# Kernel tuning notes

Measured on AMD Instinct MI355X. Metric: run time of the kernel, lower is better.

The kernel has to match this reference:

```python
import jax, jax.numpy as jnp
import numpy as np
from jax import lax

B, N, S, NS = 2, 16384, 4096, 32  # batch, points, fps samples, neighbors per ball
RADIUS = 0.08
C_IN = 64
MLP_DIMS = [3 + C_IN, 64, 64, 128]


def setup_inputs() -> dict:
    key = jax.random.key(0)
    ks = jax.random.split(key, 8)
    xyz = jax.random.uniform(ks[0], (B, N, 3), jnp.float32)  # unit cube point cloud
    features = jax.random.normal(ks[1], (B, C_IN, N), jnp.float32)
    inp = {"xyz": xyz, "features": features}
    for i in range(3):
        inp[f"W{i}"] = jax.random.normal(ks[2 + i], (MLP_DIMS[i + 1], MLP_DIMS[i]), jnp.float32) * 0.05
        inp[f"b{i}"] = jnp.zeros((MLP_DIMS[i + 1],), jnp.float32)
    return inp


def _furthest_point_sample(xyz, npoint):
    # Iterative FPS, vectorized over batch; sequential over npoint via lax.scan.
    b, n, _ = xyz.shape
    init_idx = jnp.zeros((b,), jnp.int32)

    def step(carry, _):
        min_d, last_idx = carry
        last = jnp.take_along_axis(xyz, last_idx[:, None, None], axis=1)  # (B,1,3)
        d = jnp.sum((xyz - last) ** 2, axis=-1)  # (B,N)
        min_d = jnp.minimum(min_d, d)
        nxt = jnp.argmax(min_d, axis=-1).astype(jnp.int32)
        return (min_d, nxt), nxt

    init_d = jnp.full((b, n), 1e10, xyz.dtype)
    _, rest = lax.scan(step, (init_d, init_idx), None, length=npoint - 1)
    return jnp.concatenate([init_idx[None, :], rest], axis=0).T  # (B, npoint)


def _ball_query(xyz, new_xyz, radius, nsample):
    # For each query, the first `nsample` points (by index order) within radius,
    # padded with the first found index (matches CUDA ball_query semantics).
    n = xyz.shape[1]
    d2 = jnp.sum((new_xyz[:, :, None, :] - xyz[:, None, :, :]) ** 2, axis=-1)  # (B,S,N)
    valid = d2 < radius * radius
    cnt = valid.sum(axis=-1)  # (B,S)
    keyidx = jnp.where(valid, jnp.arange(n, dtype=jnp.int32), n)
    _, idx = lax.top_k(-keyidx, nsample)  # smallest valid indices first
    idx = idx.astype(jnp.int32)
    slot_valid = jnp.arange(nsample) < cnt[..., None]
    idx = jnp.where(slot_valid, idx, idx[..., :1])
    return idx, cnt


def reference(xyz, features, W0, b0, W1, b1, W2, b2):
    fps_idx = _furthest_point_sample(xyz, S)  # (B,S)
    new_xyz = jnp.take_along_axis(xyz, fps_idx[..., None], axis=1)  # (B,S,3)

    idx, cnt = _ball_query(xyz, new_xyz, RADIUS, NS)  # (B,S,NS), (B,S)
    grouped_xyz = jax.vmap(lambda p, i: p[i])(xyz, idx)  # (B,S,NS,3)
    rel = (grouped_xyz - new_xyz[:, :, None, :]).transpose(0, 3, 1, 2)  # (B,3,S,NS)
    grouped_feat = jax.vmap(lambda f, i: f[:, i])(features, idx)  # (B,C,S,NS)
    x = jnp.concatenate([rel, grouped_feat], axis=1)  # (B,3+C,S,NS)

    for W, b in ((W0, b0), (W1, b1), (W2, b2)):  # shared MLP = 1x1 conv + ReLU
        x = jax.nn.relu(jnp.einsum('oc,bcsn->bosn', W, x) + b[None, :, None, None])

    mask = (cnt > 0).astype(x.dtype)[:, None, :, None]  # zero out empty balls
    x = x * mask
    new_features = x.max(axis=-1)  # masked max-pool over neighbors -> (B,128,S)
    return new_xyz, new_features
```

## Files before the change

### kernel.cpp

```cpp
#include <hip/hip_runtime.h>

#pragma clang fp contract(off)

#define BATCH 2
#define NPTS  16384
#define SS    4096
#define NSAMP 32
#define CIN   64

__global__ __launch_bounds__(256) void prep_kernel(
    const float* __restrict__ feat, const float* __restrict__ W0,
    float* __restrict__ ftr, float* __restrict__ W0p)
{
    __shared__ float tl[64][65];
    const int t = threadIdx.x;
    const int blk = blockIdx.x;
    if (blk < BATCH * (NPTS / 64)) {
        const int b  = blk / (NPTS / 64);
        const int n0 = (blk % (NPTS / 64)) * 64;
        #pragma unroll
        for (int k = 0; k < 16; ++k) {
            int c = k * 4 + (t >> 6);
            int n = t & 63;
            tl[c][n] = feat[((size_t)b * CIN + c) * NPTS + n0 + n];
        }
        __syncthreads();
        #pragma unroll
        for (int k = 0; k < 16; ++k) {
            int n = k * 4 + (t >> 6);
            int c = t & 63;
            ftr[((size_t)b * NPTS + n0 + n) * CIN + c] = tl[c][n];
        }
    } else {
        for (int i = t; i < 64 * 68; i += 256) {
            int r = i / 68, c = i % 68;
            W0p[i] = (c < 67) ? W0[r * 67 + c] : 0.f;
        }
    }
}

__global__ __launch_bounds__(1024, 4) void fps_kernel(
    const float* __restrict__ xyz, float* __restrict__ newxyz)
{
    #pragma clang fp contract(off)
    const int b = blockIdx.x;
    const int t = threadIdx.x;
    const float* xb = xyz + (size_t)b * NPTS * 3;

    float px[16], py[16], pz[16], md[16];
    #pragma unroll
    for (int k = 0; k < 16; ++k) {
        int p = (k << 10) + t;
        px[k] = xb[p * 3 + 0];
        py[k] = xb[p * 3 + 1];
        pz[k] = xb[p * 3 + 2];
        md[k] = 1e10f;
    }

    __shared__ float2 s_w[2][16];

    float lx = xb[0], ly = xb[1], lz = xb[2];
    if (t == 0) {
        float* o = newxyz + (size_t)b * SS * 3;
        o[0] = lx; o[1] = ly; o[2] = lz;
    }

    for (int s = 1; s < SS; ++s) {
        float bv = -1.f;
        int bi = 0;
        #pragma unroll
        for (int k = 0; k < 16; ++k) {
            float dx = px[k] - lx, dy = py[k] - ly, dz = pz[k] - lz;
            float d = (dx * dx + dy * dy) + dz * dz;
            float m = md[k];
            m = d < m ? d : m;
            md[k] = m;
            if (m > bv) { bv = m; bi = (k << 10) + t; }
        }

        #pragma unroll
        for (int m = 1; m < 64; m <<= 1) {
            float ov = __shfl_xor(bv, m);
            int   oi = __shfl_xor(bi, m);
            bool take = (ov > bv) || (ov == bv && oi < bi);
            if (take) { bv = ov; bi = oi; }
        }

        const int pb = s & 1;
        if ((t & 63) == 0)
            s_w[pb][t >> 6] = make_float2(bv, __int_as_float(bi));
        __syncthreads();

        float2 rw = s_w[pb][t & 15];
        float rv = rw.x;
        int   ri = __float_as_int(rw.y);
        #pragma unroll
        for (int m = 1; m < 16; m <<= 1) {
            float ov = __shfl_xor(rv, m);
            int   oi = __shfl_xor(ri, m);
            bool take = (ov > rv) || (ov == rv && oi < ri);
            if (take) { rv = ov; ri = oi; }
        }

        const int wi = __builtin_amdgcn_readfirstlane(ri);
        lx = xb[wi * 3 + 0];
        ly = xb[wi * 3 + 1];
        lz = xb[wi * 3 + 2];
        if (t == 0) {
            float* o = newxyz + ((size_t)b * SS + s) * 3;
            o[0] = lx; o[1] = ly; o[2] = lz;
        }
    }
}

__global__ __launch_bounds__(256) void bq_kernel(
    const float* __restrict__ xyz, const float* __restrict__ newxyz,
    int* __restrict__ idxout, int* __restrict__ cntout)
{
    #pragma clang fp contract(off)
    const int lane = threadIdx.x & 63;
    const int q = blockIdx.x * 4 + (threadIdx.x >> 6);
    const int b = q >> 12;
    const float r2 = (float)(0.08 * 0.08);
    const float cx = newxyz[q * 3 + 0];
    const float cy = newxyz[q * 3 + 1];
    const float cz = newxyz[q * 3 + 2];
    const float* xb = xyz + (size_t)b * NPTS * 3;

    int found = 0;
    int idx0 = 0;
    for (int base = 0; base < NPTS; base += 64) {
        int p = base + lane;
        float dx = xb[p * 3 + 0] - cx;
        float dy = xb[p * 3 + 1] - cy;
        float dz = xb[p * 3 + 2] - cz;
        float d2 = (dx * dx + dy * dy) + dz * dz;
        bool valid = d2 < r2;
        unsigned long long mask = __ballot(valid);
        if (mask) {
            if (found == 0) idx0 = base + (__ffsll(mask) - 1);
            int rank = found + __popcll(mask & ((1ull << lane) - 1ull));
            if (valid && rank < NSAMP) idxout[(size_t)q * NSAMP + rank] = p;
            found += (int)__popcll(mask);
            if (found >= NSAMP) break;
        }
    }
    if (found < NSAMP) {
        int pad = (found > 0) ? idx0 : 0;
        if (found + lane < NSAMP) idxout[(size_t)q * NSAMP + found + lane] = pad;
    }
    if (lane == 0) cntout[q] = found;
}

__global__ __launch_bounds__(128) void mlp_kernel(
    const float* __restrict__ xyz, const float* __restrict__ newxyz,
    const float* __restrict__ ftr, const int* __restrict__ idxbuf,
    const int* __restrict__ cntbuf, const float* __restrict__ W0p,
    const float* __restrict__ b0, const float* __restrict__ W1,
    const float* __restrict__ b1, const float* __restrict__ W2,
    const float* __restrict__ b2, float* __restrict__ outfeat)
{
    __shared__ float sX[2][68 * 36];
    __shared__ float sY[2][64 * 36];
    const int w    = threadIdx.x >> 6;
    const int lane = threadIdx.x & 63;
    const int g = blockIdx.x * 2 + w;
    const int b = g >> 12;
    const int s = g & (SS - 1);
    float* X = sX[w];
    float* Y = sY[w];

    const int n = lane & 31, h = lane >> 5;
    const int pidx = idxbuf[(size_t)g * NSAMP + n];
    const float cx = newxyz[g * 3 + 0];
    const float cy = newxyz[g * 3 + 1];
    const float cz = newxyz[g * 3 + 2];

    if (h == 0) {
        const float* p = xyz + ((size_t)b * NPTS + pidx) * 3;
        X[0 * 36 + n] = p[0] - cx;
        X[1 * 36 + n] = p[1] - cy;
        X[2 * 36 + n] = p[2] - cz;
        X[67 * 36 + n] = 0.f;
    }
    {
        const float4* f4 = (const float4*)(ftr + ((size_t)b * NPTS + pidx) * CIN + h * 32);
        #pragma unroll
        for (int j = 0; j < 8; ++j) {
            float4 v = f4[j];
            int c = 3 + h * 32 + j * 4;
            X[(c + 0) * 36 + n] = v.x;
            X[(c + 1) * 36 + n] = v.y;
            X[(c + 2) * 36 + n] = v.z;
            X[(c + 3) * 36 + n] = v.w;
        }
    }
    __syncthreads();

    const int og = lane >> 3, ng = lane & 7;

    float acc0[8][4];
    #pragma unroll
    for (int j = 0; j < 8; ++j)
        #pragma unroll
        for (int nn = 0; nn < 4; ++nn) acc0[j][nn] = 0.f;
    for (int cb = 0; cb < 17; ++cb) {
        const int c = cb * 4;
        float4 xr0 = *(const float4*)&X[(c + 0) * 36 + ng * 4];
        float4 xr1 = *(const float4*)&X[(c + 1) * 36 + ng * 4];
        float4 xr2 = *(const float4*)&X[(c + 2) * 36 + ng * 4];
        float4 xr3 = *(const float4*)&X[(c + 3) * 36 + ng * 4];
        #pragma unroll
        for (int j = 0; j < 8; ++j) {
            float4 wv = *(const float4*)&W0p[(size_t)(og * 8 + j) * 68 + c];
            acc0[j][0] = fmaf(wv.x, xr0.x, acc0[j][0]);
            acc0[j][1] = fmaf(wv.x, xr0.y, acc0[j][1]);
            acc0[j][2] = fmaf(wv.x, xr0.z, acc0[j][2]);
            acc0[j][3] = fmaf(wv.x, xr0.w, acc0[j][3]);
            acc0[j][0] = fmaf(wv.y, xr1.x, acc0[j][0]);
            acc0[j][1] = fmaf(wv.y, xr1.y, acc0[j][1]);
            acc0[j][2] = fmaf(wv.y, xr1.z, acc0[j][2]);
            acc0[j][3] = fmaf(wv.y, xr1.w, acc0[j][3]);
            acc0[j][0] = fmaf(wv.z, xr2.x, acc0[j][0]);
            acc0[j][1] = fmaf(wv.z, xr2.y, acc0[j][1]);
            acc0[j][2] = fmaf(wv.z, xr2.z, acc0[j][2]);
            acc0[j][3] = fmaf(wv.z, xr2.w, acc0[j][3]);
            acc0[j][0] = fmaf(wv.w, xr3.x, acc0[j][0]);
            acc0[j][1] = fmaf(wv.w, xr3.y, acc0[j][1]);
            acc0[j][2] = fmaf(wv.w, xr3.z, acc0[j][2]);
            acc0[j][3] = fmaf(wv.w, xr3.w, acc0[j][3]);
        }
    }
    #pragma unroll
    for (int j = 0; j < 8; ++j) {
        const float bv = b0[og * 8 + j];
        float4 yv;
        yv.x = fmaxf(acc0[j][0] + bv, 0.f);
        yv.y = fmaxf(acc0[j][1] + bv, 0.f);
        yv.z = fmaxf(acc0[j][2] + bv, 0.f);
        yv.w = fmaxf(acc0[j][3] + bv, 0.f);
        *(float4*)&Y[(og * 8 + j) * 36 + ng * 4] = yv;
    }
    __syncthreads();

    float acc1[8][4];
    #pragma unroll
    for (int j = 0; j < 8; ++j)
        #pragma unroll
        for (int nn = 0; nn < 4; ++nn) acc1[j][nn] = 0.f;
    for (int cb = 0; cb < 16; ++cb) {
        const int c = cb * 4;
        float4 xr0 = *(const float4*)&Y[(c + 0) * 36 + ng * 4];
        float4 xr1 = *(const float4*)&Y[(c + 1) * 36 + ng * 4];
        float4 xr2 = *(const float4*)&Y[(c + 2) * 36 + ng * 4];
        float4 xr3 = *(const float4*)&Y[(c + 3) * 36 + ng * 4];
        #pragma unroll
        for (int j = 0; j < 8; ++j) {
            float4 wv = *(const float4*)&W1[(size_t)(og * 8 + j) * 64 + c];
            acc1[j][0] = fmaf(wv.x, xr0.x, acc1[j][0]);
            acc1[j][1] = fmaf(wv.x, xr0.y, acc1[j][1]);
            acc1[j][2] = fmaf(wv.x, xr0.z, acc1[j][2]);
            acc1[j][3] = fmaf(wv.x, xr0.w, acc1[j][3]);
            acc1[j][0] = fmaf(wv.y, xr1.x, acc1[j][0]);
            acc1[j][1] = fmaf(wv.y, xr1.y, acc1[j][1]);
            acc1[j][2] = fmaf(wv.y, xr1.z, acc1[j][2]);
            acc1[j][3] = fmaf(wv.y, xr1.w, acc1[j][3]);
            acc1[j][0] = fmaf(wv.z, xr2.x, acc1[j][0]);
            acc1[j][1] = fmaf(wv.z, xr2.y, acc1[j][1]);
            acc1[j][2] = fmaf(wv.z, xr2.z, acc1[j][2]);
            acc1[j][3] = fmaf(wv.z, xr2.w, acc1[j][3]);
            acc1[j][0] = fmaf(wv.w, xr3.x, acc1[j][0]);
            acc1[j][1] = fmaf(wv.w, xr3.y, acc1[j][1]);
            acc1[j][2] = fmaf(wv.w, xr3.z, acc1[j][2]);
            acc1[j][3] = fmaf(wv.w, xr3.w, acc1[j][3]);
        }
    }
    __syncthreads();
    #pragma unroll
    for (int j = 0; j < 8; ++j) {
        const float bv = b1[og * 8 + j];
        float4 yv;
        yv.x = fmaxf(acc1[j][0] + bv, 0.f);
        yv.y = fmaxf(acc1[j][1] + bv, 0.f);
        yv.z = fmaxf(acc1[j][2] + bv, 0.f);
        yv.w = fmaxf(acc1[j][3] + bv, 0.f);
        *(float4*)&X[(og * 8 + j) * 36 + ng * 4] = yv;
    }
    __syncthreads();

    float acc2[16][4];
    #pragma unroll
    for (int j = 0; j < 16; ++j)
        #pragma unroll
        for (int nn = 0; nn < 4; ++nn) acc2[j][nn] = 0.f;
    for (int cb = 0; cb < 16; ++cb) {
        const int c = cb * 4;
        float4 xr0 = *(const float4*)&X[(c + 0) * 36 + ng * 4];
        float4 xr1 = *(const float4*)&X[(c + 1) * 36 + ng * 4];
        float4 xr2 = *(const float4*)&X[(c + 2) * 36 + ng * 4];
        float4 xr3 = *(const float4*)&X[(c + 3) * 36 + ng * 4];
        #pragma unroll
        for (int j = 0; j < 16; ++j) {
            float4 wv = *(const float4*)&W2[(size_t)(og * 16 + j) * 64 + c];
            acc2[j][0] = fmaf(wv.x, xr0.x, acc2[j][0]);
            acc2[j][1] = fmaf(wv.x, xr0.y, acc2[j][1]);
            acc2[j][2] = fmaf(wv.x, xr0.z, acc2[j][2]);
            acc2[j][3] = fmaf(wv.x, xr0.w, acc2[j][3]);
            acc2[j][0] = fmaf(wv.y, xr1.x, acc2[j][0]);
            acc2[j][1] = fmaf(wv.y, xr1.y, acc2[j][1]);
            acc2[j][2] = fmaf(wv.y, xr1.z, acc2[j][2]);
            acc2[j][3] = fmaf(wv.y, xr1.w, acc2[j][3]);
            acc2[j][0] = fmaf(wv.z, xr2.x, acc2[j][0]);
            acc2[j][1] = fmaf(wv.z, xr2.y, acc2[j][1]);
            acc2[j][2] = fmaf(wv.z, xr2.z, acc2[j][2]);
            acc2[j][3] = fmaf(wv.z, xr2.w, acc2[j][3]);
            acc2[j][0] = fmaf(wv.w, xr3.x, acc2[j][0]);
            acc2[j][1] = fmaf(wv.w, xr3.y, acc2[j][1]);
            acc2[j][2] = fmaf(wv.w, xr3.z, acc2[j][2]);
            acc2[j][3] = fmaf(wv.w, xr3.w, acc2[j][3]);
        }
    }

    const int cnt = cntbuf[g];
    const float msk = (cnt > 0) ? 1.f : 0.f;
    float* ob = outfeat + ((size_t)b * 128) * SS + s;
    float mj[16];
    #pragma unroll
    for (int j = 0; j < 16; ++j) {
        const float bv = b2[og * 16 + j];
        float v0 = fmaxf(acc2[j][0] + bv, acc2[j][1] + bv);
        float v1 = fmaxf(acc2[j][2] + bv, acc2[j][3] + bv);
        float v = fmaxf(fmaxf(v0, v1), 0.f);
        v = fmaxf(v, __shfl_xor(v, 1));
        v = fmaxf(v, __shfl_xor(v, 2));
        v = fmaxf(v, __shfl_xor(v, 4));
        mj[j] = v * msk;
    }
    if (ng == 0) {
        #pragma unroll
        for (int j = 0; j < 16; ++j)
            ob[(size_t)(og * 16 + j) * SS] = mj[j];
    }
}

extern "C" void kernel_launch(void* const* d_in, const int* in_sizes, int n_in,
                              void* d_out, int out_size, void* d_ws, size_t ws_size,
                              hipStream_t stream)
{
    (void)in_sizes; (void)n_in; (void)out_size; (void)ws_size;
    const float* xyz  = (const float*)d_in[0];
    const float* feat = (const float*)d_in[1];
    const float* W0 = (const float*)d_in[2];
    const float* b0 = (const float*)d_in[3];
    const float* W1 = (const float*)d_in[4];
    const float* b1 = (const float*)d_in[5];
    const float* W2 = (const float*)d_in[6];
    const float* b2 = (const float*)d_in[7];

    float* out     = (float*)d_out;
    float* newxyz  = out;
    float* outfeat = out + (size_t)BATCH * SS * 3;

    char* ws = (char*)d_ws;
    float* ftr = (float*)ws;
    size_t off = (size_t)BATCH * NPTS * CIN * sizeof(float);
    int* idxbuf = (int*)(ws + off); off += (size_t)BATCH * SS * NSAMP * sizeof(int);
    int* cntbuf = (int*)(ws + off); off += (size_t)BATCH * SS * sizeof(int);
    float* W0p  = (float*)(ws + off);

    prep_kernel<<<dim3(BATCH * (NPTS / 64) + 1), dim3(256), 0, stream>>>(feat, W0, ftr, W0p);
    fps_kernel<<<dim3(BATCH), dim3(1024), 0, stream>>>(xyz, newxyz);
    bq_kernel<<<dim3(BATCH * SS / 4), dim3(256), 0, stream>>>(xyz, newxyz, idxbuf, cntbuf);
    mlp_kernel<<<dim3(BATCH * SS / 2), dim3(128), 0, stream>>>(
        xyz, newxyz, ftr, idxbuf, cntbuf, W0p, b0, W1, b1, W2, b2, outfeat);
}
```

Before: 8.851 ms.

## Split FPS across 8 cooperating blocks per batch with global atomic argmax slots

Furthest point sampling now runs on eight workgroups per batch element instead of one, each holding two points per thread. Each iteration the blocks publish a packed (distance, inverted index) key to a global slot array with release stores and spin on acquire loads until all eight have posted, then take the maximum. This shortens the per-iteration compute and spreads the work over more CUs, at the cost of a cross-block global-memory handshake in every one of the 4095 steps. It relies on all 16 blocks being co-resident and needs a memset of the slot buffer before launch.

```diff
diff --git a/kernel.cpp b/kernel.cpp
--- a/kernel.cpp
+++ b/kernel.cpp
@@ -7,6 +7,7 @@
 #define SS    4096
 #define NSAMP 32
 #define CIN   64
+#define GPB   8
 
 __global__ __launch_bounds__(256) void prep_kernel(
     const float* __restrict__ feat, const float* __restrict__ W0,
@@ -39,77 +40,98 @@
     }
 }
 
-__global__ __launch_bounds__(1024, 4) void fps_kernel(
-    const float* __restrict__ xyz, float* __restrict__ newxyz)
+__global__ __launch_bounds__(1024) void fps_kernel(
+    const float* __restrict__ xyz, float* __restrict__ newxyz,
+    unsigned long long* __restrict__ slots)
 {
     #pragma clang fp contract(off)
-    const int b = blockIdx.x;
-    const int t = threadIdx.x;
+    const int blk = blockIdx.x;
+    const int b   = blk >> 3;
+    const int g   = blk & (GPB - 1);
+    const int t   = threadIdx.x;
     const float* xb = xyz + (size_t)b * NPTS * 3;
-
-    float px[16], py[16], pz[16], md[16];
-    #pragma unroll
-    for (int k = 0; k < 16; ++k) {
-        int p = (k << 10) + t;
-        px[k] = xb[p * 3 + 0];
-        py[k] = xb[p * 3 + 1];
-        pz[k] = xb[p * 3 + 2];
-        md[k] = 1e10f;
-    }
-
-    __shared__ float2 s_w[2][16];
+    unsigned long long* sb = slots + (size_t)b * SS * GPB;
+
+    const int p0 = (g << 11) + (t << 1);
+    const int p1 = p0 + 1;
+    float x0 = xb[p0 * 3 + 0], y0 = xb[p0 * 3 + 1], z0 = xb[p0 * 3 + 2];
+    float x1 = xb[p1 * 3 + 0], y1 = xb[p1 * 3 + 1], z1 = xb[p1 * 3 + 2];
+    float md0 = 1e10f, md1 = 1e10f;
+
+    __shared__ float2 s_w[16];
+    __shared__ float  s_c[3];
 
     float lx = xb[0], ly = xb[1], lz = xb[2];
-    if (t == 0) {
+    if (g == 0 && t == 0) {
         float* o = newxyz + (size_t)b * SS * 3;
         o[0] = lx; o[1] = ly; o[2] = lz;
     }
 
     for (int s = 1; s < SS; ++s) {
-        float bv = -1.f;
-        int bi = 0;
-        #pragma unroll
-        for (int k = 0; k < 16; ++k) {
-            float dx = px[k] - lx, dy = py[k] - ly, dz = pz[k] - lz;
-            float d = (dx * dx + dy * dy) + dz * dz;
-            float m = md[k];
-            m = d < m ? d : m;
-            md[k] = m;
-            if (m > bv) { bv = m; bi = (k << 10) + t; }
-        }
+        float dx0 = x0 - lx, dy0 = y0 - ly, dz0 = z0 - lz;
+        float d0 = (dx0 * dx0 + dy0 * dy0) + dz0 * dz0;
+        md0 = d0 < md0 ? d0 : md0;
+        float dx1 = x1 - lx, dy1 = y1 - ly, dz1 = z1 - lz;
+        float d1 = (dx1 * dx1 + dy1 * dy1) + dz1 * dz1;
+        md1 = d1 < md1 ? d1 : md1;
+
+        float bv = md1 > md0 ? md1 : md0;
+        int   bi = md1 > md0 ? p1 : p0;
 
         #pragma unroll
         for (int m = 1; m < 64; m <<= 1) {
             float ov = __shfl_xor(bv, m);
             int   oi = __shfl_xor(bi, m);
-            bool take = (ov > bv) || (ov == bv && oi < bi);
-            if (take) { bv = ov; bi = oi; }
-        }
-
-        const int pb = s & 1;
-        if ((t & 63) == 0)
-            s_w[pb][t >> 6] = make_float2(bv, __int_as_float(bi));
+            bool tk = (ov > bv) || (ov == bv && oi < bi);
+            if (tk) { bv = ov; bi = oi; }
+        }
+        if ((t & 63) == 0) s_w[t >> 6] = make_float2(bv, __int_as_float(bi));
         __syncthreads();
 
-        float2 rw = s_w[pb][t & 15];
-        float rv = rw.x;
-        int   ri = __float_as_int(rw.y);
-        #pragma unroll
-        for (int m = 1; m < 16; m <<= 1) {
-            float ov = __shfl_xor(rv, m);
-            int   oi = __shfl_xor(ri, m);
-            bool take = (ov > rv) || (ov == rv && oi < ri);
-            if (take) { rv = ov; ri = oi; }
-        }
-
-        const int wi = __builtin_amdgcn_readfirstlane(ri);
-        lx = xb[wi * 3 + 0];
-        ly = xb[wi * 3 + 1];
-        lz = xb[wi * 3 + 2];
-        if (t == 0) {
-            float* o = newxyz + ((size_t)b * SS + s) * 3;
-            o[0] = lx; o[1] = ly; o[2] = lz;
-        }
+        if (t < 64) {
+            float2 rw = s_w[t & 15];
+            float rv = rw.x;
+            int   ri = __float_as_int(rw.y);
+            #pragma unroll
+            for (int m = 1; m < 16; m <<= 1) {
+                float ov = __shfl_xor(rv, m);
+                int   oi = __shfl_xor(ri, m);
+                bool tk = (ov > rv) || (ov == rv && oi < ri);
+                if (tk) { rv = ov; ri = oi; }
+            }
+            if (t == 0) {
+                unsigned long long key =
+                    ((unsigned long long)__float_as_uint(rv) << 32) |
+                    (unsigned long long)(0xFFFFFFFFu - (unsigned)ri);
+                __hip_atomic_store(&sb[(size_t)s * GPB + g], key,
+                                   __ATOMIC_RELEASE, __HIP_MEMORY_SCOPE_AGENT);
+                unsigned long long best;
+                for (;;) {
+                    best = 0ull;
+                    bool all = true;
+                    #pragma unroll
+                    for (int j = 0; j < GPB; ++j) {
+                        unsigned long long kk = __hip_atomic_load(
+                            &sb[(size_t)s * GPB + j],
+                            __ATOMIC_ACQUIRE, __HIP_MEMORY_SCOPE_AGENT);
+                        all = all && (kk != 0ull);
+                        best = kk > best ? kk : best;
+                    }
+                    if (all) break;
+                }
+                const int wi = (int)(0xFFFFFFFFu - (unsigned)best);
+                float wx = xb[wi * 3 + 0];
+                float wy = xb[wi * 3 + 1];
+                float wz = xb[wi * 3 + 2];
+                s_c[0] = wx; s_c[1] = wy; s_c[2] = wz;
+                if (g == 0) {
+                    float* o = newxyz + ((size_t)b * SS + s) * 3;
+                    o[0] = wx; o[1] = wy; o[2] = wz;
+                }
+            }
+        }
+        __syncthreads();
+        lx = s_c[0]; ly = s_c[1]; lz = s_c[2];
     }
 }
 
@@ -366,10 +388,13 @@
     size_t off = (size_t)BATCH * NPTS * CIN * sizeof(float);
     int* idxbuf = (int*)(ws + off); off += (size_t)BATCH * SS * NSAMP * sizeof(int);
     int* cntbuf = (int*)(ws + off); off += (size_t)BATCH * SS * sizeof(int);
-    float* W0p  = (float*)(ws + off);
-
+    float* W0p  = (float*)(ws + off); off += 64 * 68 * sizeof(float);
+    unsigned long long* slots = (unsigned long long*)(ws + off);
+    const size_t slots_bytes = (size_t)BATCH * SS * GPB * sizeof(unsigned long long);
+
+    hipMemsetAsync(slots, 0, slots_bytes, stream);
     prep_kernel<<<dim3(BATCH * (NPTS / 64) + 1), dim3(256), 0, stream>>>(feat, W0, ftr, W0p);
-    fps_kernel<<<dim3(BATCH), dim3(1024), 0, stream>>>(xyz, newxyz);
+    fps_kernel<<<dim3(BATCH * GPB), dim3(1024), 0, stream>>>(xyz, newxyz, slots);
     bq_kernel<<<dim3(BATCH * SS / 4), dim3(256), 0, stream>>>(xyz, newxyz, idxbuf, cntbuf);
     mlp_kernel<<<dim3(BATCH * SS / 2), dim3(128), 0, stream>>>(
         xyz, newxyz, ftr, idxbuf, cntbuf, W0p, b0, W1, b1, W2, b2, outfeat);
```

Result: slower. 16.05 ms (+81.3%).
